# Kernel tuning notes

Measured on AMD Instinct MI355X. Metric: run time of the kernel, lower is better.

## Reference

```python
import jax, jax.numpy as jnp
import numpy as np

RATE = 5          # negative_sample_rate
A = 1.0           # _a
BP = 1.0          # _b
REP = 1.0         # repulsion_strength
EPS = 1e-4        # clamp in compute_cross_entropy
BATCH = 65536; C = 100; E = 2048; GN = 16; GP = 5; NIDX = 50000


def setup_inputs() -> dict:
    key = jax.random.key(0)
    ks = jax.random.split(key, 12)
    return {
        'edge_to_idx': jax.random.randint(ks[0], (BATCH,), 0, NIDX),
        'edge_from_idx': jax.random.randint(ks[1], (BATCH,), 0, NIDX),
        'embedding_to': jax.random.normal(ks[2], (BATCH, 2), jnp.float32),
        'embedding_from': jax.random.normal(ks[3], (BATCH, 2), jnp.float32),
        'probs': jax.random.uniform(ks[4], (BATCH,), jnp.float32),
        'pred_edge_to': jax.random.normal(ks[5], (BATCH, C), jnp.float32),
        'pred_edge_from': jax.random.normal(ks[6], (BATCH, C), jnp.float32),
        'perm': jax.random.permutation(ks[7], BATCH * RATE),            # torch.randperm
        'error_conf': jnp.sort(jax.random.randint(ks[8], (E,), 0, NIDX)),
        'neg_grid': jax.random.normal(ks[9], (E, GN, 2), jnp.float32),
        'pos_grid': jax.random.normal(ks[10], (E, GP, 2), jnp.float32),
        'distance_list': jax.random.uniform(ks[11], (E,), jnp.float32),
    }


def _q(d):
    # convert_distance_to_probability: 1 / (1 + a * d^(2b))
    return 1.0 / (1.0 + A * d ** (2.0 * BP))


def _ce_attract(p, q):
    return -p * jnp.log(jnp.clip(q, EPS, 1.0))


def _ce_repulse(p, q):
    return -(1.0 - p) * REP * jnp.log(jnp.clip(1.0 - q, EPS, 1.0))


def _match(idx, error_conf):
    # first position in (sorted) error_conf equal to idx, plus hit mask
    pos = jnp.clip(jnp.searchsorted(error_conf, idx), 0, error_conf.shape[0] - 1)
    return pos, (error_conf[pos] == idx)


def reference(edge_to_idx, edge_from_idx, embedding_to, embedding_from, probs,
              pred_edge_to, pred_edge_from, perm, error_conf, neg_grid,
              pos_grid, distance_list):
    f32 = jnp.float32
    # ---- negative sampling (repeat_interleave + randperm) ----
    emb_neg_to = jnp.repeat(embedding_to, RATE, axis=0)         # [B*R,2]
    pred_neg_to = jnp.repeat(pred_edge_to, RATE, axis=0)        # [B*R,C]
    emb_neg_from = jnp.repeat(embedding_from, RATE, axis=0)[perm]
    pred_neg_from = jnp.repeat(pred_edge_from, RATE, axis=0)[perm]
    # filter_neg: keep where NOT (same argmax AND same max-softmax confidence)
    conf_from = jnp.max(jax.nn.softmax(pred_neg_from, axis=1), axis=1)
    conf_to = jnp.max(jax.nn.softmax(pred_neg_to, axis=1), axis=1)
    same = (jnp.argmax(pred_neg_from, axis=1) == jnp.argmax(pred_neg_to, axis=1)) & (conf_from == conf_to)
    m_neg = (~same).astype(f32)                                 # [B*R]
    neg_dist = jnp.linalg.norm(emb_neg_to - emb_neg_from, axis=1)
    neg_cnt = jnp.sum(m_neg)
    neg_mean = jnp.sum(neg_dist * m_neg) / jnp.maximum(neg_cnt, 1.0)
    # ---- positive distances ----
    pos_dist = jnp.linalg.norm(embedding_to - embedding_from, axis=1)  # [B]
    pos_mean = jnp.mean(pos_dist)
    # ---- confidence-grid pairs (vectorized isin/nonzero loops) ----
    g_to, hit_to = _match(edge_to_idx, error_conf)
    g_from, hit_from = _match(edge_from_idx, error_conf)
    m_to = hit_to.astype(f32)
    m_from = hit_from.astype(f32)
    d_cneg_to = jnp.linalg.norm(embedding_to[:, None, :] - neg_grid[g_to], axis=-1)     # [B,GN]
    d_cneg_from = jnp.linalg.norm(embedding_from[:, None, :] - neg_grid[g_from], axis=-1)
    d_cpos_to = jnp.linalg.norm(embedding_from[:, None, :] - pos_grid[g_to], axis=-1)   # [B,GP]
    d_cpos_from = jnp.linalg.norm(embedding_from[:, None, :] - pos_grid[g_from], axis=-1)
    w_pos_to = m_to * (distance_list[g_to] < 0.5).astype(f32)
    w_pos_from = m_from * (distance_list[g_from] < 1.0).astype(f32)
    # ---- UMAP cross entropy over the concatenated (pos, conf_pos, neg, conf_neg) ----
    ce_pos = _ce_attract(probs, _q(pos_dist)) + _ce_repulse(probs, _q(pos_dist))
    sum_ce = jnp.sum(ce_pos)
    sum_ce += jnp.sum(w_pos_to[:, None] * _ce_attract(1.0, _q(d_cpos_to)))
    sum_ce += jnp.sum(w_pos_from[:, None] * _ce_attract(1.0, _q(d_cpos_from)))
    sum_ce += jnp.sum(m_neg * _ce_repulse(0.0, _q(neg_dist)))
    sum_ce += jnp.sum(m_to[:, None] * _ce_repulse(0.0, _q(d_cneg_to)))
    sum_ce += jnp.sum(m_from[:, None] * _ce_repulse(0.0, _q(d_cneg_from)))
    total_cnt = (pos_dist.shape[0] + GP * (jnp.sum(w_pos_to) + jnp.sum(w_pos_from))
                 + neg_cnt + GN * (jnp.sum(m_to) + jnp.sum(m_from)))
    umap_l = sum_ce / jnp.maximum(total_cnt, 1.0)
    umap_l = jnp.where(jnp.isnan(umap_l), 0.0, umap_l)
    # ---- margin loss ----
    is_pred_same = (jnp.argmax(pred_edge_to, axis=1) == jnp.argmax(pred_edge_from, axis=1)).astype(f32)
    batch_margin = pos_mean + (neg_mean - pos_mean) * (1.0 - probs)
    margin = (1.0 - is_pred_same) * batch_margin
    margin_loss = jnp.mean(jax.nn.relu(margin - pos_dist))
    margin_loss = jnp.where(jnp.isnan(margin_loss), 0.0, margin_loss)
    return (umap_l, margin_loss, umap_l + margin_loss)


if __name__ == '__main__':
    out = reference(**setup_inputs())
    print([float(o) for o in out])
```

## Files before the change

### kernel.cpp

```cpp
#include <hip/hip_runtime.h>
#include <math.h>

#define B_SZ   65536
#define RATE   5
#define NNEG   (B_SZ * RATE)
#define NC     100
#define NE     2048
#define GN     16
#define GP     5
#define EPSC   1e-4f

#define NBN    1280
#define NBP    256
#define NBT    256

__device__ __forceinline__ float wave_sumf(float v) {
    #pragma unroll
    for (int off = 32; off > 0; off >>= 1) v += __shfl_down(v, off, 64);
    return v;
}
__device__ __forceinline__ float clip01(float x) {
    return fminf(fmaxf(x, EPSC), 1.0f);
}

__global__ __launch_bounds__(256, 2) void k_rowstats(
    const float* __restrict__ pred_to, const float* __restrict__ pred_from,
    float2* __restrict__ pk_to, float2* __restrict__ pk_from,
    unsigned int* __restrict__ counter)
{
    if (blockIdx.x == 0 && threadIdx.x == 0) *counter = 0u;
    int i = blockIdx.x * blockDim.x + threadIdx.x;
    const float* row = (i < B_SZ) ? pred_to + (size_t)i * NC
                                  : pred_from + (size_t)(i - B_SZ) * NC;
    const float4* r4 = (const float4*)row;
    float4 v[25];
    #pragma unroll
    for (int t = 0; t < 25; ++t) v[t] = r4[t];

    float m = -INFINITY;
    #pragma unroll
    for (int t = 0; t < 25; ++t)
        m = fmaxf(m, fmaxf(fmaxf(v[t].x, v[t].y), fmaxf(v[t].z, v[t].w)));

    int bi = NC;
    float s = 0.0f;
    #pragma unroll
    for (int t = 0; t < 25; ++t) {
        float e0 = v[t].x, e1 = v[t].y, e2 = v[t].z, e3 = v[t].w;
        if (e0 == m) bi = min(bi, 4 * t + 0);
        if (e1 == m) bi = min(bi, 4 * t + 1);
        if (e2 == m) bi = min(bi, 4 * t + 2);
        if (e3 == m) bi = min(bi, 4 * t + 3);
        s += expf(e0 - m) + expf(e1 - m) + expf(e2 - m) + expf(e3 - m);
    }
    float2 pk = make_float2(1.0f / s, __uint_as_float((unsigned)bi));
    if (i < B_SZ) pk_to[i] = pk; else pk_from[i - B_SZ] = pk;
}

__global__ __launch_bounds__(256) void k_negpos(
    const int* __restrict__ perm,
    const float2* __restrict__ emb_to, const float2* __restrict__ emb_from,
    const float2* __restrict__ pk_to, const float2* __restrict__ pk_from,
    const int* __restrict__ idx_to, const int* __restrict__ idx_from,
    const float* __restrict__ probs,
    const int* __restrict__ error_conf,
    const float2* __restrict__ neg_grid, const float2* __restrict__ pos_grid,
    const float* __restrict__ dist_list,
    float* __restrict__ pneg, float* __restrict__ ppos)
{
    __shared__ float sr[6][4];
    int w = threadIdx.x >> 6, lane = threadIdx.x & 63;
    if (blockIdx.x < NBN) {
        const unsigned long long* pkt = (const unsigned long long*)pk_to;
        const unsigned long long* pkf = (const unsigned long long*)pk_from;
        int i = blockIdx.x * 256 + threadIdx.x;
        float ce = 0.f, cnt = 0.f, ds = 0.f;
        {
            unsigned jt = (unsigned)i / RATE;
            unsigned jf = (unsigned)perm[i] / RATE;
            if (pkt[jt] != pkf[jf]) {
                float2 et = emb_to[jt], ef = emb_from[jf];
                float dx = et.x - ef.x, dy = et.y - ef.y;
                float d2 = dx * dx + dy * dy;
                float om = d2 / (1.0f + d2);
                ce  = -logf(clip01(om));
                cnt = 1.0f;
                ds  = sqrtf(d2);
            }
        }
        ce = wave_sumf(ce); cnt = wave_sumf(cnt); ds = wave_sumf(ds);
        if (lane == 0) { sr[0][w] = ce; sr[1][w] = cnt; sr[2][w] = ds; }
        __syncthreads();
        if (threadIdx.x < 3) {
            int j = threadIdx.x;
            pneg[blockIdx.x * 3 + j] = sr[j][0] + sr[j][1] + sr[j][2] + sr[j][3];
        }
    } else {
        __shared__ int ec[NE];
        int blk = blockIdx.x - NBN;
        for (int t = threadIdx.x; t < NE; t += 256) ec[t] = error_conf[t];
        __syncthreads();

        float v0 = 0.f, v1 = 0.f, v2 = 0.f, v3 = 0.f, v4 = 0.f, v5 = 0.f;
        {
            int i = blk * 256 + threadIdx.x;
            float2 et = emb_to[i], ef = emb_from[i];
            float dx = et.x - ef.x, dy = et.y - ef.y;
            float d2 = dx * dx + dy * dy;
            v1 = sqrtf(d2);
            float p = probs[i];
            float q  = 1.0f / (1.0f + d2);
            float om = d2 / (1.0f + d2);
            v0 = -p * logf(clip01(q)) - (1.0f - p) * logf(clip01(om));

            int vt = idx_to[i];
            int lo = 0, hi = NE;
            while (lo < hi) { int mid = (lo + hi) >> 1; if (ec[mid] < vt) lo = mid + 1; else hi = mid; }
            int gt = (lo < NE) ? lo : NE - 1;
            bool hit_t = (ec[gt] == vt);

            int vf = idx_from[i];
            lo = 0; hi = NE;
            while (lo < hi) { int mid = (lo + hi) >> 1; if (ec[mid] < vf) lo = mid + 1; else hi = mid; }
            int gf = (lo < NE) ? lo : NE - 1;
            bool hit_f = (ec[gf] == vf);

            if (hit_t) {
                v4 = 1.0f;
                float sa = 0.f;
                #pragma unroll
                for (int k2 = 0; k2 < GN; ++k2) {
                    float2 g = neg_grid[gt * GN + k2];
                    float ax = et.x - g.x, ay = et.y - g.y;
                    float dd = ax * ax + ay * ay;
                    sa += -logf(clip01(dd / (1.0f + dd)));
                }
                v0 += sa;
                if (dist_list[gt] < 0.5f) {
                    v2 = 1.0f;
                    float s2 = 0.f;
                    #pragma unroll
                    for (int k2 = 0; k2 < GP; ++k2) {
                        float2 g = pos_grid[gt * GP + k2];
                        float ax = ef.x - g.x, ay = ef.y - g.y;
                        float dd = ax * ax + ay * ay;
                        s2 += -logf(clip01(1.0f / (1.0f + dd)));
                    }
                    v0 += s2;
                }
            }
            if (hit_f) {
                v5 = 1.0f;
                float sa = 0.f;
                #pragma unroll
                for (int k2 = 0; k2 < GN; ++k2) {
                    float2 g = neg_grid[gf * GN + k2];
                    float ax = ef.x - g.x, ay = ef.y - g.y;
                    float dd = ax * ax + ay * ay;
                    sa += -logf(clip01(dd / (1.0f + dd)));
                }
                v0 += sa;
                if (dist_list[gf] < 1.0f) {
                    v3 = 1.0f;
                    float s2 = 0.f;
                    #pragma unroll
                    for (int k2 = 0; k2 < GP; ++k2) {
                        float2 g = pos_grid[gf * GP + k2];
                        float ax = ef.x - g.x, ay = ef.y - g.y;
                        float dd = ax * ax + ay * ay;
                        s2 += -logf(clip01(1.0f / (1.0f + dd)));
                    }
                    v0 += s2;
                }
            }
        }
        float vv[6] = {v0, v1, v2, v3, v4, v5};
        #pragma unroll
        for (int j = 0; j < 6; ++j) {
            float r = wave_sumf(vv[j]);
            if (lane == 0) sr[j][w] = r;
        }
        __syncthreads();
        if (threadIdx.x < 6) {
            int j = threadIdx.x;
            ppos[blk * 6 + j] = sr[j][0] + sr[j][1] + sr[j][2] + sr[j][3];
        }
    }
}

__global__ __launch_bounds__(256) void k_tail(
    const float2* __restrict__ emb_to, const float2* __restrict__ emb_from,
    const float* __restrict__ probs,
    const float2* __restrict__ pk_to, const float2* __restrict__ pk_from,
    const float* __restrict__ pneg, const float* __restrict__ ppos,
    float* __restrict__ pmar, unsigned int* __restrict__ counter,
    float* __restrict__ out)
{
    __shared__ float sr[8][4];
    __shared__ float tot[8];
    __shared__ bool islast;
    int w = threadIdx.x >> 6, lane = threadIdx.x & 63;

    float s[8] = {0, 0, 0, 0, 0, 0, 0, 0};
    for (int b = threadIdx.x; b < NBN; b += 256) {
        s[0] += pneg[b * 3 + 0]; s[1] += pneg[b * 3 + 1]; s[2] += pneg[b * 3 + 2];
    }
    for (int b = threadIdx.x; b < NBP; b += 256) {
        s[0] += ppos[b * 6 + 0]; s[3] += ppos[b * 6 + 1]; s[4] += ppos[b * 6 + 2];
        s[5] += ppos[b * 6 + 3]; s[6] += ppos[b * 6 + 4]; s[7] += ppos[b * 6 + 5];
    }
    #pragma unroll
    for (int j = 0; j < 8; ++j) {
        float r = wave_sumf(s[j]);
        if (lane == 0) sr[j][w] = r;
    }
    __syncthreads();
    if (threadIdx.x < 8) {
        int j = threadIdx.x;
        tot[j] = sr[j][0] + sr[j][1] + sr[j][2] + sr[j][3];
    }
    __syncthreads();
    float pos_mean = tot[3] * (1.0f / (float)B_SZ);
    float neg_mean = tot[2] / fmaxf(tot[1], 1.0f);

    int i = blockIdx.x * 256 + threadIdx.x;
    float2 et = emb_to[i], ef = emb_from[i];
    float2 at = pk_to[i], af = pk_from[i];
    float dx = et.x - ef.x, dy = et.y - ef.y;
    float d = sqrtf(dx * dx + dy * dy);
    float p = probs[i];
    float bm = pos_mean + (neg_mean - pos_mean) * (1.0f - p);
    float mg = (at.y == af.y) ? 0.0f : bm;
    float ms = fmaxf(mg - d, 0.0f);
    ms = wave_sumf(ms);
    if (lane == 0) sr[0][w] = ms;
    __syncthreads();

    if (threadIdx.x == 0) {
        pmar[blockIdx.x] = sr[0][0] + sr[0][1] + sr[0][2] + sr[0][3];
        __threadfence();
        unsigned old = atomicAdd(counter, 1u);
        islast = (old == NBT - 1);
    }
    __syncthreads();
    if (islast) {
        __threadfence();
        float v = pmar[threadIdx.x];
        v = wave_sumf(v);
        if (lane == 0) sr[1][w] = v;
        __syncthreads();
        if (threadIdx.x == 0) {
            float msum = sr[1][0] + sr[1][1] + sr[1][2] + sr[1][3];
            float total_cnt = (float)B_SZ + (float)GP * (tot[4] + tot[5])
                            + tot[1] + (float)GN * (tot[6] + tot[7]);
            float umap = tot[0] / fmaxf(total_cnt, 1.0f);
            if (isnan(umap)) umap = 0.0f;
            float ml = msum * (1.0f / (float)B_SZ);
            if (isnan(ml)) ml = 0.0f;
            out[0] = umap;
            out[1] = ml;
            out[2] = umap + ml;
        }
    }
}

extern "C" void kernel_launch(void* const* d_in, const int* in_sizes, int n_in,
                              void* d_out, int out_size, void* d_ws, size_t ws_size,
                              hipStream_t stream)
{
    const int*   edge_to_idx   = (const int*)d_in[0];
    const int*   edge_from_idx = (const int*)d_in[1];
    const float* embedding_to  = (const float*)d_in[2];
    const float* embedding_from= (const float*)d_in[3];
    const float* probs         = (const float*)d_in[4];
    const float* pred_to       = (const float*)d_in[5];
    const float* pred_from     = (const float*)d_in[6];
    const int*   perm          = (const int*)d_in[7];
    const int*   error_conf    = (const int*)d_in[8];
    const float* neg_grid      = (const float*)d_in[9];
    const float* pos_grid      = (const float*)d_in[10];
    const float* dist_list     = (const float*)d_in[11];

    char* ws = (char*)d_ws;
    unsigned int* counter = (unsigned int*)ws;
    float2*       pk_to   = (float2*)(ws + 256);
    float2*       pk_from = pk_to + B_SZ;
    float*        pneg    = (float*)(pk_from + B_SZ);
    float*        ppos    = pneg + NBN * 3;
    float*        pmar    = ppos + NBP * 6;

    k_rowstats<<<(2 * B_SZ) / 256, 256, 0, stream>>>(
        pred_to, pred_from, pk_to, pk_from, counter);

    k_negpos<<<NBN + NBP, 256, 0, stream>>>(
        perm, (const float2*)embedding_to, (const float2*)embedding_from,
        pk_to, pk_from,
        edge_to_idx, edge_from_idx, probs, error_conf,
        (const float2*)neg_grid, (const float2*)pos_grid, dist_list,
        pneg, ppos);

    k_tail<<<NBT, 256, 0, stream>>>(
        (const float2*)embedding_to, (const float2*)embedding_from,
        probs, pk_to, pk_from, pneg, ppos, pmar, counter, (float*)d_out);
}
```

Before: 43.89 us.

## Split row softmax/argmax across 16 lanes with shuffle reductions for coalesced loads

The row-stats kernel now assigns each 100-float prediction row to 16 lanes instead of one thread. Each lane loads one or two float4s, and the max, argmax and exp-sum are reduced with width-16 xor shuffles. This makes adjacent lanes read contiguous memory, removes the 25-float4 per-thread register array, and launches 16x more threads. The cost is the extra shuffle reductions. A variable in the other kernel is renamed to avoid a name clash.

New measurement: 44.37 us. No clear change (+1.1%).

```diff
diff --git a/kernel.cpp b/kernel.cpp
--- a/kernel.cpp
+++ b/kernel.cpp
@@ -29,32 +29,44 @@
     unsigned int* __restrict__ counter)
 {
     if (blockIdx.x == 0 && threadIdx.x == 0) *counter = 0u;
-    int i = blockIdx.x * blockDim.x + threadIdx.x;
-    const float* row = (i < B_SZ) ? pred_to + (size_t)i * NC
-                                  : pred_from + (size_t)(i - B_SZ) * NC;
-    const float4* r4 = (const float4*)row;
-    float4 v[25];
-    #pragma unroll
-    for (int t = 0; t < 25; ++t) v[t] = r4[t];
-
-    float m = -INFINITY;
-    #pragma unroll
-    for (int t = 0; t < 25; ++t)
-        m = fmaxf(m, fmaxf(fmaxf(v[t].x, v[t].y), fmaxf(v[t].z, v[t].w)));
+    int gt  = blockIdx.x * 256 + threadIdx.x;
+    int wid = gt >> 4;
+    int col = gt & 15;
+    const float* row = (wid < B_SZ) ? pred_to + (size_t)wid * NC
+                                    : pred_from + (size_t)(wid - B_SZ) * NC;
+    float4 a = ((const float4*)row)[col];
+    float4 b;
+    bool hasb = (col < 9);
+    if (hasb) b = ((const float4*)row)[16 + col];
+    else      b = make_float4(-INFINITY, -INFINITY, -INFINITY, -INFINITY);
+
+    float m = fmaxf(fmaxf(a.x, a.y), fmaxf(a.z, a.w));
+    m = fmaxf(m, fmaxf(fmaxf(b.x, b.y), fmaxf(b.z, b.w)));
+    #pragma unroll
+    for (int mk = 1; mk < 16; mk <<= 1) m = fmaxf(m, __shfl_xor(m, mk, 16));
 
     int bi = NC;
-    float s = 0.0f;
-    #pragma unroll
-    for (int t = 0; t < 25; ++t) {
-        float e0 = v[t].x, e1 = v[t].y, e2 = v[t].z, e3 = v[t].w;
-        if (e0 == m) bi = min(bi, 4 * t + 0);
-        if (e1 == m) bi = min(bi, 4 * t + 1);
-        if (e2 == m) bi = min(bi, 4 * t + 2);
-        if (e3 == m) bi = min(bi, 4 * t + 3);
-        s += expf(e0 - m) + expf(e1 - m) + expf(e2 - m) + expf(e3 - m);
-    }
-    float2 pk = make_float2(1.0f / s, __uint_as_float((unsigned)bi));
-    if (i < B_SZ) pk_to[i] = pk; else pk_from[i - B_SZ] = pk;
+    int i0 = 4 * col, i1 = 64 + 4 * col;
+    if (a.x == m) bi = min(bi, i0 + 0);
+    if (a.y == m) bi = min(bi, i0 + 1);
+    if (a.z == m) bi = min(bi, i0 + 2);
+    if (a.w == m) bi = min(bi, i0 + 3);
+    if (b.x == m) bi = min(bi, i1 + 0);
+    if (b.y == m) bi = min(bi, i1 + 1);
+    if (b.z == m) bi = min(bi, i1 + 2);
+    if (b.w == m) bi = min(bi, i1 + 3);
+    #pragma unroll
+    for (int mk = 1; mk < 16; mk <<= 1) bi = min(bi, __shfl_xor(bi, mk, 16));
+
+    float s = expf(a.x - m) + expf(a.y - m) + expf(a.z - m) + expf(a.w - m)
+            + expf(b.x - m) + expf(b.y - m) + expf(b.z - m) + expf(b.w - m);
+    #pragma unroll
+    for (int mk = 1; mk < 16; mk <<= 1) s += __shfl_xor(s, mk, 16);
+
+    if (col == 0) {
+        float2 pk = make_float2(1.0f / s, __uint_as_float((unsigned)bi));
+        if (wid < B_SZ) pk_to[wid] = pk; else pk_from[wid - B_SZ] = pk;
+    }
 }
 
 __global__ __launch_bounds__(256) void k_negpos(
@@ -116,8 +128,8 @@
             int vt = idx_to[i];
             int lo = 0, hi = NE;
             while (lo < hi) { int mid = (lo + hi) >> 1; if (ec[mid] < vt) lo = mid + 1; else hi = mid; }
-            int gt = (lo < NE) ? lo : NE - 1;
-            bool hit_t = (ec[gt] == vt);
+            int gtd = (lo < NE) ? lo : NE - 1;
+            bool hit_t = (ec[gtd] == vt);
 
             int vf = idx_from[i];
             lo = 0; hi = NE;
@@ -130,18 +142,18 @@
                 float sa = 0.f;
                 #pragma unroll
                 for (int k2 = 0; k2 < GN; ++k2) {
-                    float2 g = neg_grid[gt * GN + k2];
+                    float2 g = neg_grid[gtd * GN + k2];
                     float ax = et.x - g.x, ay = et.y - g.y;
                     float dd = ax * ax + ay * ay;
                     sa += -logf(clip01(dd / (1.0f + dd)));
                 }
                 v0 += sa;
-                if (dist_list[gt] < 0.5f) {
+                if (dist_list[gtd] < 0.5f) {
                     v2 = 1.0f;
                     float s2 = 0.f;
                     #pragma unroll
                     for (int k2 = 0; k2 < GP; ++k2) {
-                        float2 g = pos_grid[gt * GP + k2];
+                        float2 g = pos_grid[gtd * GP + k2];
                         float ax = ef.x - g.x, ay = ef.y - g.y;
                         float dd = ax * ax + ay * ay;
                         s2 += -logf(clip01(1.0f / (1.0f + dd)));
@@ -289,7 +301,7 @@
     float*        ppos    = pneg + NBN * 3;
     float*        pmar    = ppos + NBP * 6;
 
-    k_rowstats<<<(2 * B_SZ) / 256, 256, 0, stream>>>(
+    k_rowstats<<<(2 * B_SZ * 16) / 256, 256, 0, stream>>>(
         pred_to, pred_from, pk_to, pk_from, counter);
 
     k_negpos<<<NBN + NBP, 256, 0, stream>>>(
```
